# Kernel optimization log

Measured on AMD Instinct MI355X. Metric: run time of the kernel, lower is better.

Reference implementation:

```python
import jax, jax.numpy as jnp
import numpy as np

BN_EPS = 1e-5
HEADS = 8

def _bn(y, gamma, beta, mean, var):
    # eval-mode BatchNorm2d over channel axis 1; y: [B,C,H,W]
    scale = gamma / jnp.sqrt(var + BN_EPS)
    shift = beta - mean * scale
    return y * scale[None, :, None, None] + shift[None, :, None, None]

def setup_inputs() -> dict:
    key = jax.random.key(0)
    ks = jax.random.split(key, 12)
    B, C, H, W = 16, 256, 64, 64
    x = jax.random.normal(ks[0], (B, C, H, W), jnp.float32)
    qkv_w = jax.random.normal(ks[1], (3 * C, C), jnp.float32) * 0.05
    qkv_gamma = jax.random.uniform(ks[2], (3 * C,), jnp.float32, 0.5, 1.5)
    qkv_beta = jax.random.normal(ks[3], (3 * C,), jnp.float32) * 0.1
    qkv_mean = jax.random.normal(ks[4], (3 * C,), jnp.float32) * 0.1
    qkv_var = jax.random.uniform(ks[5], (3 * C,), jnp.float32, 0.5, 1.5)
    proj_w = jax.random.normal(ks[6], (C, C), jnp.float32) * 0.05
    proj_gamma = jax.random.uniform(ks[7], (C,), jnp.float32, 0.5, 1.5)
    proj_beta = jax.random.normal(ks[8], (C,), jnp.float32) * 0.1
    proj_mean = jax.random.normal(ks[9], (C,), jnp.float32) * 0.1
    proj_var = jax.random.uniform(ks[10], (C,), jnp.float32, 0.5, 1.5)
    return {"x": x, "qkv_w": qkv_w, "qkv_gamma": qkv_gamma, "qkv_beta": qkv_beta,
            "qkv_mean": qkv_mean, "qkv_var": qkv_var, "proj_w": proj_w,
            "proj_gamma": proj_gamma, "proj_beta": proj_beta,
            "proj_mean": proj_mean, "proj_var": proj_var}

def reference(x, qkv_w, qkv_gamma, qkv_beta, qkv_mean, qkv_var,
              proj_w, proj_gamma, proj_beta, proj_mean, proj_var):
    B, C, H, W = x.shape
    hd = C // HEADS  # head_dim
    # 1x1 conv (no bias) + BN
    qkv = jnp.einsum('bchw,oc->bohw', x, qkv_w)
    qkv = _bn(qkv, qkv_gamma, qkv_beta, qkv_mean, qkv_var)
    q, k, v = jnp.split(qkv, 3, axis=1)
    N = H * W
    q = q.reshape(B, HEADS, hd, N)
    k = k.reshape(B, HEADS, hd, N)
    v = v.reshape(B, HEADS, hd, N)
    q = jax.nn.softmax(q, axis=-1)   # over tokens
    k = jax.nn.softmax(k, axis=-2)   # over head_dim
    context = jnp.einsum('bhdn,bhen->bhde', k, v)   # [B,h,d,d]
    out = jnp.einsum('bhdn,bhde->bhen', q, context) # [B,h,d,N]
    out = out.reshape(B, C, H, W)
    out = jnp.einsum('bchw,oc->bohw', out, proj_w)
    out = _bn(out, proj_gamma, proj_beta, proj_mean, proj_var)
    return out
```

## Files before the change

kernel.cpp:

```cpp
#include <hip/hip_runtime.h>

typedef unsigned short ushort_t;
typedef unsigned int u32;
typedef short short8 __attribute__((ext_vector_type(8)));
typedef short short4_t __attribute__((ext_vector_type(4)));
typedef float f32x4 __attribute__((ext_vector_type(4)));
typedef float f32x16 __attribute__((ext_vector_type(16)));

#define NTOK 4096
#define NCOLS 65536
#define CIN 256

__device__ __forceinline__ float b2f(ushort_t u) {
    union { unsigned int i; float f; } v; v.i = ((unsigned int)u) << 16; return v.f;
}
__device__ __forceinline__ ushort_t f2b(float f) {
    union { float f; unsigned int i; } v; v.f = f;
    unsigned int r = v.i + 0x7FFFu + ((v.i >> 16) & 1u);
    return (ushort_t)(r >> 16);
}

__device__ __forceinline__ void gl_lds16(const ushort_t* g, ushort_t* l) {
    __builtin_amdgcn_global_load_lds(
        (const __attribute__((address_space(1))) u32*)(const void*)g,
        (__attribute__((address_space(3))) u32*)(void*)l,
        16, 0, 0);
}

__global__ __launch_bounds__(256) void cvt_w(const float* __restrict__ wq,
                                             const float* __restrict__ wp,
                                             ushort_t* __restrict__ wqb,
                                             ushort_t* __restrict__ wpb,
                                             float* __restrict__ scz) {
    int i = blockIdx.x * 256 + threadIdx.x;
    if (i < 768 * 256) wqb[i] = f2b(wq[i]);
    else               wpb[i - 768 * 256] = f2b(wp[i - 768 * 256]);
    if (i < 131072) scz[i] = 0.f;
}

__global__ __launch_bounds__(256) void transpose_x(const float* __restrict__ x,
                                                   ushort_t* __restrict__ xt) {
    __shared__ ushort_t lds[64 * 264];
    int tid = threadIdx.x;
    int g0 = blockIdx.x * 64;
    int b = g0 >> 12, n0 = g0 & 4095;
    const float* src = x + (size_t)b * (CIN * NTOK);
    int tn = tid & 63, cg = tid >> 6;
    for (int c4 = 0; c4 < 64; c4++) {
        int c = c4 * 4 + cg;
        lds[tn * 264 + c] = f2b(src[(size_t)c * NTOK + n0 + tn]);
    }
    __syncthreads();
    int tok = tid >> 2, c8 = (tid & 3) * 8;
    ushort_t* dst = xt + (size_t)(g0 + tok) * CIN + c8;
#pragma unroll
    for (int j = 0; j < 8; j++)
        *(short8*)(dst + j * 32) = *(const short8*)&lds[tok * 264 + c8 + j * 32];
}

__global__ __launch_bounds__(256) void gemm128(const ushort_t* __restrict__ W,
                                               const ushort_t* __restrict__ Xc,
                                               const float* __restrict__ gamma,
                                               const float* __restrict__ beta,
                                               const float* __restrict__ mean,
                                               const float* __restrict__ var,
                                               ushort_t* __restrict__ out_b,
                                               float* __restrict__ out_f, int mode) {
    __shared__ __align__(16) ushort_t lA[128 * 32];
    __shared__ __align__(16) ushort_t lB[128 * 32];
    int tid = threadIdx.x;
    int wave = tid >> 6, lane = tid & 63;
    int l15 = lane & 15, q = lane >> 4;
    int mh = wave >> 1, nh = wave & 1;
    int m0 = blockIdx.y * 128, colb = blockIdx.x * 128;

    f32x4 acc[4][4];
#pragma unroll
    for (int i = 0; i < 4; i++)
#pragma unroll
        for (int j = 0; j < 4; j++)
#pragma unroll
            for (int r = 0; r < 4; r++) acc[i][j][r] = 0.f;

    const ushort_t* gA0 = W  + (size_t)(m0 +      (tid >> 2)) * CIN + (tid & 3) * 8;
    const ushort_t* gA1 = W  + (size_t)(m0 + 64 + (tid >> 2)) * CIN + (tid & 3) * 8;
    const ushort_t* gB0 = Xc + (size_t)(colb +      (tid >> 2)) * CIN + (tid & 3) * 8;
    const ushort_t* gB1 = Xc + (size_t)(colb + 64 + (tid >> 2)) * CIN + (tid & 3) * 8;
    ushort_t* la0 = &lA[tid * 8];
    ushort_t* la1 = &lA[2048 + tid * 8];
    ushort_t* lb0 = &lB[tid * 8];
    ushort_t* lb1 = &lB[2048 + tid * 8];

    for (int k0 = 0; k0 < CIN; k0 += 32) {
        gl_lds16(gA0 + k0, la0);
        gl_lds16(gA1 + k0, la1);
        gl_lds16(gB0 + k0, lb0);
        gl_lds16(gB1 + k0, lb1);
        __syncthreads();
        short8 af[4], bf[4];
#pragma unroll
        for (int i = 0; i < 4; i++) {
            af[i] = *(const short8*)&lA[(mh * 64 + i * 16 + l15) * 32 + q * 8];
            bf[i] = *(const short8*)&lB[(nh * 64 + i * 16 + l15) * 32 + q * 8];
        }
#pragma unroll
        for (int mi = 0; mi < 4; mi++)
#pragma unroll
            for (int ni = 0; ni < 4; ni++)
                acc[mi][ni] = __builtin_amdgcn_mfma_f32_16x16x32_bf16(af[mi], bf[ni],
                                                                      acc[mi][ni], 0, 0, 0);
        __syncthreads();
    }

    int col_l = colb + nh * 64 + l15;
#pragma unroll
    for (int mi = 0; mi < 4; mi++) {
#pragma unroll
        for (int r = 0; r < 4; r++) {
            int m = m0 + mh * 64 + mi * 16 + q * 4 + r;
            float sc = gamma[m] * rsqrtf(var[m] + 1e-5f);
            float sh = beta[m] - mean[m] * sc;
#pragma unroll
            for (int ni = 0; ni < 4; ni++) {
                float val = acc[mi][ni][r] * sc + sh;
                int col = col_l + ni * 16;
                if (mode == 0) {
                    out_b[(size_t)m * NCOLS + col] = f2b(val);
                } else {
                    int bb = col >> 12, n = col & 4095;
                    out_f[(size_t)bb * (CIN * NTOK) + (size_t)m * NTOK + n] = val;
                }
            }
        }
    }
}

__global__ __launch_bounds__(256) void qsum_ker(const ushort_t* __restrict__ qkv,
                                                float* __restrict__ qsums) {
    int tid = threadIdx.x, wave = tid >> 6, lane = tid & 63;
    int rid = blockIdx.x * 4 + wave;
    int c = rid >> 4, b = rid & 15;
    const ushort_t* row = qkv + (size_t)c * NCOLS + b * NTOK;
    float s = 0.f;
#pragma unroll
    for (int j = 0; j < 8; j++) {
        short8 pk = *(const short8*)(row + j * 512 + lane * 8);
#pragma unroll
        for (int i = 0; i < 8; i++) s += __expf(b2f((ushort_t)pk[i]));
    }
    for (int off = 1; off < 64; off <<= 1) s += __shfl_xor(s, off);
    if (lane == 0) qsums[c * 16 + b] = s;
}

__global__ __launch_bounds__(256) void ctx_ker(const ushort_t* __restrict__ qkv,
                                               float* __restrict__ ctxbuf) {
    int sl = blockIdx.x, bh = blockIdx.y;
    int b = bh >> 3, h = bh & 7;
    int tid = threadIdx.x, wave = tid >> 6, lane = tid & 63;
    int l31 = lane & 31, l5 = lane >> 5;
    int col0 = b * NTOK + sl * 512 + wave * 128;
    const ushort_t* krow = qkv + (size_t)(256 + h * 32 + l31) * NCOLS + col0 + l5 * 8;
    const ushort_t* vrow = qkv + (size_t)(512 + h * 32 + l31) * NCOLS + col0 + l5 * 8;
    f32x16 acc;
#pragma unroll
    for (int i = 0; i < 16; i++) acc[i] = 0.f;
#pragma unroll
    for (int st = 0; st < 8; st++) {
        short8 kf = *(const short8*)(krow + st * 16);
        short8 vf = *(const short8*)(vrow + st * 16);
        short8 af;
#pragma unroll
        for (int j = 0; j < 8; j++) {
            float e = __expf(b2f((ushort_t)kf[j]));
            float t = e;
            t += __shfl_xor(t, 1);
            t += __shfl_xor(t, 2);
            t += __shfl_xor(t, 4);
            t += __shfl_xor(t, 8);
            t += __shfl_xor(t, 16);
            af[j] = (short)f2b(__fdividef(e, t));
        }
        acc = __builtin_amdgcn_mfma_f32_32x32x16_bf16(af, vf, acc, 0, 0, 0);
    }
    __shared__ float red[4][1024];
#pragma unroll
    for (int r = 0; r < 16; r++) {
        int d = (r & 3) + 8 * (r >> 2) + 4 * l5;
        red[wave][d * 32 + l31] = acc[r];
    }
    __syncthreads();
    int i0 = tid * 4;
#pragma unroll
    for (int i = 0; i < 4; i++) {
        int idx = i0 + i;
        float v = red[0][idx] + red[1][idx] + red[2][idx] + red[3][idx];
        atomicAdd(ctxbuf + (size_t)bh * 1024 + idx, v);
    }
}

__global__ __launch_bounds__(256) void out_ker(const ushort_t* __restrict__ qkv,
                                               const float* __restrict__ ctxbuf,
                                               const float* __restrict__ qsums,
                                               ushort_t* __restrict__ attT) {
    int sl = blockIdx.x, bh = blockIdx.y;
    int b = bh >> 3, h = bh & 7;
    int tid = threadIdx.x, wave = tid >> 6, lane = tid & 63;
    int l31 = lane & 31, l5 = lane >> 5;
    __shared__ __align__(16) ushort_t ctxT[32 * 40];
    __shared__ __align__(16) ushort_t qT[256 * 40];
    __shared__ __align__(16) ushort_t obuf[4][32 * 40];

#pragma unroll
    for (int i = 0; i < 4; i++) {
        int idx = tid * 4 + i;
        int d = idx >> 5, e = idx & 31;
        ctxT[e * 40 + d] = f2b(ctxbuf[(size_t)bh * 1024 + idx]);
    }
    __syncthreads();
    short8 a0 = *(const short8*)(ctxT + l31 * 40 + l5 * 8);
    short8 a1 = *(const short8*)(ctxT + l31 * 40 + 16 + l5 * 8);

    const ushort_t* qbase = qkv + (size_t)(h * 32) * NCOLS;
    int segbase = b * NTOK + sl * 512;
    int d = tid & 31, t8 = (tid >> 5) * 8;
    float sq = 1.f / qsums[(h * 32 + d) * 16 + b];

    for (int nc = 0; nc < 2; nc++) {
        int gcol0 = segbase + nc * 256;
#pragma unroll
        for (int jj = 0; jj < 4; jj++) {
            int tok8 = jj * 64 + t8;
            short8 pk = *(const short8*)(qbase + (size_t)d * NCOLS + gcol0 + tok8);
#pragma unroll
            for (int j = 0; j < 8; j++)
                qT[(tok8 + j) * 40 + d] = f2b(__expf(b2f((ushort_t)pk[j])) * sq);
        }
        __syncthreads();
#pragma unroll
        for (int ti = 0; ti < 2; ti++) {
            int tok0 = (wave + ti * 4) * 32;
            f32x16 acc;
#pragma unroll
            for (int i = 0; i < 16; i++) acc[i] = 0.f;
            short8 b0 = *(const short8*)(qT + (size_t)(tok0 + l31) * 40 + l5 * 8);
            short8 b1 = *(const short8*)(qT + (size_t)(tok0 + l31) * 40 + 16 + l5 * 8);
            acc = __builtin_amdgcn_mfma_f32_32x32x16_bf16(a0, b0, acc, 0, 0, 0);
            acc = __builtin_amdgcn_mfma_f32_32x32x16_bf16(a1, b1, acc, 0, 0, 0);
#pragma unroll
            for (int r = 0; r < 16; r++) {
                int e = (r & 3) + 8 * (r >> 2) + 4 * l5;
                obuf[wave][l31 * 40 + e] = f2b(acc[r]);
            }
            __syncthreads();
            {
                int tok = lane >> 1, half = lane & 1;
                const ushort_t* srcp = &obuf[wave][tok * 40 + half * 16];
                short8 r0 = *(const short8*)srcp;
                short8 r1 = *(const short8*)(srcp + 8);
                size_t g = (size_t)(gcol0 + tok0 + tok) * 256 + h * 32 + half * 16;
                *(short8*)(attT + g) = r0;
                *(short8*)(attT + g + 8) = r1;
            }
            __syncthreads();
        }
        __syncthreads();
    }
}

extern "C" void kernel_launch(void* const* d_in, const int* in_sizes, int n_in,
                              void* d_out, int out_size, void* d_ws, size_t ws_size,
                              hipStream_t stream) {
    const float* x          = (const float*)d_in[0];
    const float* qkv_w      = (const float*)d_in[1];
    const float* qkv_gamma  = (const float*)d_in[2];
    const float* qkv_beta   = (const float*)d_in[3];
    const float* qkv_mean   = (const float*)d_in[4];
    const float* qkv_var    = (const float*)d_in[5];
    const float* proj_w     = (const float*)d_in[6];
    const float* proj_gamma = (const float*)d_in[7];
    const float* proj_beta  = (const float*)d_in[8];
    const float* proj_mean  = (const float*)d_in[9];
    const float* proj_var   = (const float*)d_in[10];

    ushort_t* wqb = (ushort_t*)d_ws;
    ushort_t* wpb = wqb + 768 * 256;
    ushort_t* xt  = wpb + 256 * 256;
    ushort_t* qkv = xt + (size_t)NCOLS * CIN;
    float* out    = (float*)d_out;
    float* ctxbuf = (float*)d_out;
    float* qsums  = ctxbuf + 131072;

    cvt_w<<<1024, 256, 0, stream>>>(qkv_w, proj_w, wqb, wpb, ctxbuf);
    transpose_x<<<1024, 256, 0, stream>>>(x, xt);
    gemm128<<<dim3(512, 6), 256, 0, stream>>>(wqb, xt, qkv_gamma, qkv_beta,
                                              qkv_mean, qkv_var, qkv, nullptr, 0);
    qsum_ker<<<1024, 256, 0, stream>>>(qkv, qsums);
    ctx_ker<<<dim3(8, 128), 256, 0, stream>>>(qkv, ctxbuf);
    out_ker<<<dim3(8, 128), 256, 0, stream>>>(qkv, ctxbuf, qsums, xt);
    gemm128<<<dim3(512, 2), 256, 0, stream>>>(wpb, xt, proj_gamma, proj_beta,
                                              proj_mean, proj_var, nullptr, out, 1);
}
```

Before: 298.5 us.

## Keep weight tiles in registers and stage full-K activation tiles in LDS

The 1x1-conv GEMM kernel changes from a 128x128 tile that streams both operands through LDS in 32-wide K steps, with two barriers per step. It now uses 512-thread blocks covering 256 output channels. Each wave holds its whole 64xK weight slice in registers, and the block loads a full 128-token by 256-K activation tile into LDS in one shot, covering two column tiles per block. This removes the per-K-step barriers and the repeated weight reloads, at the cost of heavy register use (128 VGPRs for weight fragments plus accumulators), 64 KB of LDS per block, and no overlap between loads and MFMA work.

```diff
diff --git a/kernel.cpp b/kernel.cpp
--- a/kernel.cpp
+++ b/kernel.cpp
@@ -3,7 +3,6 @@
 typedef unsigned short ushort_t;
 typedef unsigned int u32;
 typedef short short8 __attribute__((ext_vector_type(8)));
-typedef short short4_t __attribute__((ext_vector_type(4)));
 typedef float f32x4 __attribute__((ext_vector_type(4)));
 typedef float f32x16 __attribute__((ext_vector_type(16)));
 
@@ -58,77 +57,83 @@
         *(short8*)(dst + j * 32) = *(const short8*)&lds[tok * 264 + c8 + j * 32];
 }
 
-__global__ __launch_bounds__(256) void gemm128(const ushort_t* __restrict__ W,
-                                               const ushort_t* __restrict__ Xc,
-                                               const float* __restrict__ gamma,
-                                               const float* __restrict__ beta,
-                                               const float* __restrict__ mean,
-                                               const float* __restrict__ var,
-                                               ushort_t* __restrict__ out_b,
-                                               float* __restrict__ out_f, int mode) {
-    __shared__ __align__(16) ushort_t lA[128 * 32];
-    __shared__ __align__(16) ushort_t lB[128 * 32];
+__global__ __launch_bounds__(512, 2) void gemmW(const ushort_t* __restrict__ W,
+                                                const ushort_t* __restrict__ Xc,
+                                                const float* __restrict__ gamma,
+                                                const float* __restrict__ beta,
+                                                const float* __restrict__ mean,
+                                                const float* __restrict__ var,
+                                                ushort_t* __restrict__ out_b,
+                                                float* __restrict__ out_f, int mode) {
+    __shared__ __align__(16) ushort_t lB[32768];
     int tid = threadIdx.x;
     int wave = tid >> 6, lane = tid & 63;
     int l15 = lane & 15, q = lane >> 4;
-    int mh = wave >> 1, nh = wave & 1;
-    int m0 = blockIdx.y * 128, colb = blockIdx.x * 128;
-
-    f32x4 acc[4][4];
-#pragma unroll
-    for (int i = 0; i < 4; i++)
-#pragma unroll
-        for (int j = 0; j < 4; j++)
-#pragma unroll
-            for (int r = 0; r < 4; r++) acc[i][j][r] = 0.f;
-
-    const ushort_t* gA0 = W  + (size_t)(m0 +      (tid >> 2)) * CIN + (tid & 3) * 8;
-    const ushort_t* gA1 = W  + (size_t)(m0 + 64 + (tid >> 2)) * CIN + (tid & 3) * 8;
-    const ushort_t* gB0 = Xc + (size_t)(colb +      (tid >> 2)) * CIN + (tid & 3) * 8;
-    const ushort_t* gB1 = Xc + (size_t)(colb + 64 + (tid >> 2)) * CIN + (tid & 3) * 8;
-    ushort_t* la0 = &lA[tid * 8];
-    ushort_t* la1 = &lA[2048 + tid * 8];
-    ushort_t* lb0 = &lB[tid * 8];
-    ushort_t* lb1 = &lB[2048 + tid * 8];
-
-    for (int k0 = 0; k0 < CIN; k0 += 32) {
-        gl_lds16(gA0 + k0, la0);
-        gl_lds16(gA1 + k0, la1);
-        gl_lds16(gB0 + k0, lb0);
-        gl_lds16(gB1 + k0, lb1);
-        __syncthreads();
-        short8 af[4], bf[4];
+    int mq = wave >> 1, nq = wave & 1;
+    int m0 = blockIdx.y * 256;
+    int mrow = m0 + mq * 64;
+
+    short8 afr[8][4];
+#pragma unroll
+    for (int ks = 0; ks < 8; ks++)
+#pragma unroll
+        for (int i = 0; i < 4; i++)
+            afr[ks][i] = *(const short8*)(W + (size_t)(mrow + i * 16 + l15) * CIN
+                                            + ks * 32 + q * 8);
+
+    const ushort_t* gB = Xc + (size_t)(blockIdx.x * 256 + (tid >> 2)) * CIN
+                            + (tid & 3) * 8;
+
+    for (int ct = 0; ct < 2; ct++) {
+        if (ct) __builtin_amdgcn_s_barrier();
+        const ushort_t* gBt = gB + ct * 128 * CIN;
+#pragma unroll
+        for (int ks = 0; ks < 8; ks++)
+            gl_lds16(gBt + ks * 32, &lB[ks * 4096 + tid * 8]);
+        asm volatile("s_waitcnt vmcnt(0)" ::: "memory");
+        __builtin_amdgcn_s_barrier();
+
+        f32x4 acc[4][4];
+#pragma unroll
+        for (int i = 0; i < 4; i++)
+#pragma unroll
+            for (int j = 0; j < 4; j++)
+#pragma unroll
+                for (int r = 0; r < 4; r++) acc[i][j][r] = 0.f;
+
+#pragma unroll
+        for (int ks = 0; ks < 8; ks++) {
+            short8 bf[4];
+#pragma unroll
+            for (int nj = 0; nj < 4; nj++)
+                bf[nj] = *(const short8*)&lB[ks * 4096
+                                             + (nq * 64 + nj * 16 + l15) * 32 + q * 8];
+#pragma unroll
+            for (int i = 0; i < 4; i++)
+#pragma unroll
+                for (int nj = 0; nj < 4; nj++)
+                    acc[i][nj] = __builtin_amdgcn_mfma_f32_16x16x32_bf16(
+                        afr[ks][i], bf[nj], acc[i][nj], 0, 0, 0);
+        }
+
+        int colb = blockIdx.x * 256 + ct * 128;
 #pragma unroll
         for (int i = 0; i < 4; i++) {
-            af[i] = *(const short8*)&lA[(mh * 64 + i * 16 + l15) * 32 + q * 8];
-            bf[i] = *(const short8*)&lB[(nh * 64 + i * 16 + l15) * 32 + q * 8];
-        }
-#pragma unroll
-        for (int mi = 0; mi < 4; mi++)
-#pragma unroll
-            for (int ni = 0; ni < 4; ni++)
-                acc[mi][ni] = __builtin_amdgcn_mfma_f32_16x16x32_bf16(af[mi], bf[ni],
-                                                                      acc[mi][ni], 0, 0, 0);
-        __syncthreads();
-    }
-
-    int col_l = colb + nh * 64 + l15;
-#pragma unroll
-    for (int mi = 0; mi < 4; mi++) {
-#pragma unroll
-        for (int r = 0; r < 4; r++) {
-            int m = m0 + mh * 64 + mi * 16 + q * 4 + r;
-            float sc = gamma[m] * rsqrtf(var[m] + 1e-5f);
-            float sh = beta[m] - mean[m] * sc;
-#pragma unroll
-            for (int ni = 0; ni < 4; ni++) {
-                float val = acc[mi][ni][r] * sc + sh;
-                int col = col_l + ni * 16;
-                if (mode == 0) {
-                    out_b[(size_t)m * NCOLS + col] = f2b(val);
-                } else {
-                    int bb = col >> 12, n = col & 4095;
-                    out_f[(size_t)bb * (CIN * NTOK) + (size_t)m * NTOK + n] = val;
+#pragma unroll
+            for (int r = 0; r < 4; r++) {
+                int m = mrow + i * 16 + q * 4 + r;
+                float sc = gamma[m] * rsqrtf(var[m] + 1e-5f);
+                float sh = beta[m] - mean[m] * sc;
+#pragma unroll
+                for (int nj = 0; nj < 4; nj++) {
+                    float val = acc[i][nj][r] * sc + sh;
+                    int col = colb + nq * 64 + nj * 16 + l15;
+                    if (mode == 0) {
+                        out_b[(size_t)m * NCOLS + col] = f2b(val);
+                    } else {
+                        int bb = col >> 12, n = col & 4095;
+                        out_f[(size_t)bb * (CIN * NTOK) + (size_t)m * NTOK + n] = val;
+                    }
                 }
             }
         }
@@ -292,11 +297,11 @@
 
     cvt_w<<<1024, 256, 0, stream>>>(qkv_w, proj_w, wqb, wpb, ctxbuf);
     transpose_x<<<1024, 256, 0, stream>>>(x, xt);
-    gemm128<<<dim3(512, 6), 256, 0, stream>>>(wqb, xt, qkv_gamma, qkv_beta,
-                                              qkv_mean, qkv_var, qkv, nullptr, 0);
+    gemmW<<<dim3(256, 3), 512, 0, stream>>>(wqb, xt, qkv_gamma, qkv_beta,
+                                            qkv_mean, qkv_var, qkv, nullptr, 0);
     qsum_ker<<<1024, 256, 0, stream>>>(qkv, qsums);
     ctx_ker<<<dim3(8, 128), 256, 0, stream>>>(qkv, ctxbuf);
     out_ker<<<dim3(8, 128), 256, 0, stream>>>(qkv, ctxbuf, qsums, xt);
-    gemm128<<<dim3(512, 2), 256, 0, stream>>>(wpb, xt, proj_gamma, proj_beta,
-                                              proj_mean, proj_var, nullptr, out, 1);
-}
+    gemmW<<<dim3(256, 1), 512, 0, stream>>>(wpb, xt, proj_gamma, proj_beta,
+                                            proj_mean, proj_var, nullptr, out, 1);
+}
```

After: 384.6 us. 28.8% more time.

## Fuse weight conversion into transpose and q-softmax sums into QKV GEMM epilogue

Applied to the files above, without the earlier changes.

Merges the weight-conversion kernel into the x-transpose kernel and removes the separate qsum pass. The QKV GEMM epilogue now accumulates exp of the bf16 q values, reduces across 16 lanes, and atomically adds per-row, per-batch partial sums into qsums. The zeroing range is extended so qsums is cleared by the prep kernel. This saves two launches and a full re-read of the q rows, at the cost of atomics and extra exp work inside the GEMM epilogue.

```diff
diff --git a/kernel.cpp b/kernel.cpp
--- a/kernel.cpp
+++ b/kernel.cpp
@@ -3,7 +3,6 @@
 typedef unsigned short ushort_t;
 typedef unsigned int u32;
 typedef short short8 __attribute__((ext_vector_type(8)));
-typedef short short4_t __attribute__((ext_vector_type(4)));
 typedef float f32x4 __attribute__((ext_vector_type(4)));
 typedef float f32x16 __attribute__((ext_vector_type(16)));
 
@@ -27,21 +26,21 @@
         16, 0, 0);
 }
 
-__global__ __launch_bounds__(256) void cvt_w(const float* __restrict__ wq,
-                                             const float* __restrict__ wp,
-                                             ushort_t* __restrict__ wqb,
-                                             ushort_t* __restrict__ wpb,
-                                             float* __restrict__ scz) {
-    int i = blockIdx.x * 256 + threadIdx.x;
+__global__ __launch_bounds__(256) void prep_x(const float* __restrict__ x,
+                                              ushort_t* __restrict__ xt,
+                                              const float* __restrict__ wq,
+                                              const float* __restrict__ wp,
+                                              ushort_t* __restrict__ wqb,
+                                              ushort_t* __restrict__ wpb,
+                                              float* __restrict__ scz) {
+    __shared__ ushort_t lds[64 * 264];
+    int tid = threadIdx.x;
+
+    int i = blockIdx.x * 256 + tid;
     if (i < 768 * 256) wqb[i] = f2b(wq[i]);
     else               wpb[i - 768 * 256] = f2b(wp[i - 768 * 256]);
-    if (i < 131072) scz[i] = 0.f;
-}
-
-__global__ __launch_bounds__(256) void transpose_x(const float* __restrict__ x,
-                                                   ushort_t* __restrict__ xt) {
-    __shared__ ushort_t lds[64 * 264];
-    int tid = threadIdx.x;
+    if (i < 135168) scz[i] = 0.f;
+
     int g0 = blockIdx.x * 64;
     int b = g0 >> 12, n0 = g0 & 4095;
     const float* src = x + (size_t)b * (CIN * NTOK);
@@ -65,7 +64,8 @@
                                                const float* __restrict__ mean,
                                                const float* __restrict__ var,
                                                ushort_t* __restrict__ out_b,
-                                               float* __restrict__ out_f, int mode) {
+                                               float* __restrict__ out_f,
+                                               float* __restrict__ qsums, int mode) {
     __shared__ __align__(16) ushort_t lA[128 * 32];
     __shared__ __align__(16) ushort_t lB[128 * 32];
     int tid = threadIdx.x;
@@ -113,6 +113,7 @@
     }
 
     int col_l = colb + nh * 64 + l15;
+    int bq = colb >> 12;
 #pragma unroll
     for (int mi = 0; mi < 4; mi++) {
 #pragma unroll
@@ -120,36 +121,29 @@
             int m = m0 + mh * 64 + mi * 16 + q * 4 + r;
             float sc = gamma[m] * rsqrtf(var[m] + 1e-5f);
             float sh = beta[m] - mean[m] * sc;
+            float qs = 0.f;
 #pragma unroll
             for (int ni = 0; ni < 4; ni++) {
                 float val = acc[mi][ni][r] * sc + sh;
                 int col = col_l + ni * 16;
                 if (mode == 0) {
-                    out_b[(size_t)m * NCOLS + col] = f2b(val);
+                    ushort_t bv = f2b(val);
+                    out_b[(size_t)m * NCOLS + col] = bv;
+                    if (m < 256) qs += __expf(b2f(bv));
                 } else {
                     int bb = col >> 12, n = col & 4095;
                     out_f[(size_t)bb * (CIN * NTOK) + (size_t)m * NTOK + n] = val;
                 }
             }
-        }
-    }
-}
-
-__global__ __launch_bounds__(256) void qsum_ker(const ushort_t* __restrict__ qkv,
-                                                float* __restrict__ qsums) {
-    int tid = threadIdx.x, wave = tid >> 6, lane = tid & 63;
-    int rid = blockIdx.x * 4 + wave;
-    int c = rid >> 4, b = rid & 15;
-    const ushort_t* row = qkv + (size_t)c * NCOLS + b * NTOK;
-    float s = 0.f;
-#pragma unroll
-    for (int j = 0; j < 8; j++) {
-        short8 pk = *(const short8*)(row + j * 512 + lane * 8);
-#pragma unroll
-        for (int i = 0; i < 8; i++) s += __expf(b2f((ushort_t)pk[i]));
-    }
-    for (int off = 1; off < 64; off <<= 1) s += __shfl_xor(s, off);
-    if (lane == 0) qsums[c * 16 + b] = s;
+            if (mode == 0 && m < 256) {
+                qs += __shfl_xor(qs, 1);
+                qs += __shfl_xor(qs, 2);
+                qs += __shfl_xor(qs, 4);
+                qs += __shfl_xor(qs, 8);
+                if (l15 == 0) atomicAdd(&qsums[m * 16 + bq], qs);
+            }
+        }
+    }
 }
 
 __global__ __launch_bounds__(256) void ctx_ker(const ushort_t* __restrict__ qkv,
@@ -290,13 +284,13 @@
     float* ctxbuf = (float*)d_out;
     float* qsums  = ctxbuf + 131072;
 
-    cvt_w<<<1024, 256, 0, stream>>>(qkv_w, proj_w, wqb, wpb, ctxbuf);
-    transpose_x<<<1024, 256, 0, stream>>>(x, xt);
+    prep_x<<<1024, 256, 0, stream>>>(x, xt, qkv_w, proj_w, wqb, wpb, ctxbuf);
     gemm128<<<dim3(512, 6), 256, 0, stream>>>(wqb, xt, qkv_gamma, qkv_beta,
-                                              qkv_mean, qkv_var, qkv, nullptr, 0);
-    qsum_ker<<<1024, 256, 0, stream>>>(qkv, qsums);
+                                              qkv_mean, qkv_var, qkv, nullptr,
+                                              qsums, 0);
     ctx_ker<<<dim3(8, 128), 256, 0, stream>>>(qkv, ctxbuf);
     out_ker<<<dim3(8, 128), 256, 0, stream>>>(qkv, ctxbuf, qsums, xt);
     gemm128<<<dim3(512, 2), 256, 0, stream>>>(wpb, xt, proj_gamma, proj_beta,
-                                              proj_mean, proj_var, nullptr, out, 1);
-}
+                                              proj_mean, proj_var, nullptr, out,
+                                              nullptr, 1);
+}
```

New measurement: 356.1 us. 19.3% more time.

## Precompute k-softmax reciprocals, replace context atomics with partial buffers, fuse prep kernels

Applied to the files above, without the earlier changes.

The weight conversion and x transpose kernels are merged into one prep kernel. The per-token k softmax denominators now come from extra blocks added to the q-sum kernel, which store reciprocals so ctx_ker no longer needs five shuffles and a divide per element. ctx_ker writes per-slice partial contexts instead of using atomicAdd, and out_ker sums the 8 partials, which also removes the zeroing pass. The cost is an extra pass that reads K and an extra 2 MB reciprocal buffer, plus larger scratch use in the output buffer.

```diff
diff --git a/kernel.cpp b/kernel.cpp
--- a/kernel.cpp
+++ b/kernel.cpp
@@ -3,7 +3,6 @@
 typedef unsigned short ushort_t;
 typedef unsigned int u32;
 typedef short short8 __attribute__((ext_vector_type(8)));
-typedef short short4_t __attribute__((ext_vector_type(4)));
 typedef float f32x4 __attribute__((ext_vector_type(4)));
 typedef float f32x16 __attribute__((ext_vector_type(16)));
 
@@ -27,21 +26,19 @@
         16, 0, 0);
 }
 
-__global__ __launch_bounds__(256) void cvt_w(const float* __restrict__ wq,
-                                             const float* __restrict__ wp,
-                                             ushort_t* __restrict__ wqb,
-                                             ushort_t* __restrict__ wpb,
-                                             float* __restrict__ scz) {
-    int i = blockIdx.x * 256 + threadIdx.x;
+__global__ __launch_bounds__(256) void prep_x(const float* __restrict__ x,
+                                              ushort_t* __restrict__ xt,
+                                              const float* __restrict__ wq,
+                                              const float* __restrict__ wp,
+                                              ushort_t* __restrict__ wqb,
+                                              ushort_t* __restrict__ wpb) {
+    __shared__ ushort_t lds[64 * 264];
+    int tid = threadIdx.x;
+
+    int i = blockIdx.x * 256 + tid;
     if (i < 768 * 256) wqb[i] = f2b(wq[i]);
     else               wpb[i - 768 * 256] = f2b(wp[i - 768 * 256]);
-    if (i < 131072) scz[i] = 0.f;
-}
-
-__global__ __launch_bounds__(256) void transpose_x(const float* __restrict__ x,
-                                                   ushort_t* __restrict__ xt) {
-    __shared__ ushort_t lds[64 * 264];
-    int tid = threadIdx.x;
+
     int g0 = blockIdx.x * 64;
     int b = g0 >> 12, n0 = g0 & 4095;
     const float* src = x + (size_t)b * (CIN * NTOK);
@@ -135,25 +132,50 @@
     }
 }
 
-__global__ __launch_bounds__(256) void qsum_ker(const ushort_t* __restrict__ qkv,
-                                                float* __restrict__ qsums) {
-    int tid = threadIdx.x, wave = tid >> 6, lane = tid & 63;
-    int rid = blockIdx.x * 4 + wave;
-    int c = rid >> 4, b = rid & 15;
-    const ushort_t* row = qkv + (size_t)c * NCOLS + b * NTOK;
-    float s = 0.f;
-#pragma unroll
-    for (int j = 0; j < 8; j++) {
-        short8 pk = *(const short8*)(row + j * 512 + lane * 8);
-#pragma unroll
-        for (int i = 0; i < 8; i++) s += __expf(b2f((ushort_t)pk[i]));
-    }
-    for (int off = 1; off < 64; off <<= 1) s += __shfl_xor(s, off);
-    if (lane == 0) qsums[c * 16 + b] = s;
+__global__ __launch_bounds__(256) void sum_ker(const ushort_t* __restrict__ qkv,
+                                               float* __restrict__ qsums,
+                                               float* __restrict__ rsums) {
+    int tid = threadIdx.x;
+    if (blockIdx.x < 1024) {
+        int wave = tid >> 6, lane = tid & 63;
+        int rid = blockIdx.x * 4 + wave;
+        int c = rid >> 4, b = rid & 15;
+        const ushort_t* row = qkv + (size_t)c * NCOLS + b * NTOK;
+        float s = 0.f;
+#pragma unroll
+        for (int j = 0; j < 8; j++) {
+            short8 pk = *(const short8*)(row + j * 512 + lane * 8);
+#pragma unroll
+            for (int i = 0; i < 8; i++) s += __expf(b2f((ushort_t)pk[i]));
+        }
+        for (int off = 1; off < 64; off <<= 1) s += __shfl_xor(s, off);
+        if (lane == 0) qsums[c * 16 + b] = s;
+    } else {
+        int kb = blockIdx.x - 1024;
+        int bh = kb >> 1, half = kb & 1;
+        int b = bh >> 3, h = bh & 7;
+        const ushort_t* base = qkv + (size_t)(256 + h * 32) * NCOLS
+                                   + b * NTOK + half * 2048 + tid * 8;
+        float s[8];
+#pragma unroll
+        for (int j = 0; j < 8; j++) s[j] = 0.f;
+        for (int ch = 0; ch < 32; ch++) {
+            short8 kk = *(const short8*)(base + (size_t)ch * NCOLS);
+#pragma unroll
+            for (int j = 0; j < 8; j++) s[j] += __expf(b2f((ushort_t)kk[j]));
+        }
+        float* rp = rsums + (size_t)bh * NTOK + half * 2048 + tid * 8;
+        f32x4 r0, r1;
+#pragma unroll
+        for (int j = 0; j < 4; j++) { r0[j] = 1.f / s[j]; r1[j] = 1.f / s[j + 4]; }
+        *(f32x4*)rp = r0;
+        *(f32x4*)(rp + 4) = r1;
+    }
 }
 
 __global__ __launch_bounds__(256) void ctx_ker(const ushort_t* __restrict__ qkv,
-                                               float* __restrict__ ctxbuf) {
+                                               const float* __restrict__ rsums,
+                                               float* __restrict__ ctxpart) {
     int sl = blockIdx.x, bh = blockIdx.y;
     int b = bh >> 3, h = bh & 7;
     int tid = threadIdx.x, wave = tid >> 6, lane = tid & 63;
@@ -161,6 +183,7 @@
     int col0 = b * NTOK + sl * 512 + wave * 128;
     const ushort_t* krow = qkv + (size_t)(256 + h * 32 + l31) * NCOLS + col0 + l5 * 8;
     const ushort_t* vrow = qkv + (size_t)(512 + h * 32 + l31) * NCOLS + col0 + l5 * 8;
+    const float* rsp = rsums + (size_t)bh * NTOK + sl * 512 + wave * 128 + l5 * 8;
     f32x16 acc;
 #pragma unroll
     for (int i = 0; i < 16; i++) acc[i] = 0.f;
@@ -168,18 +191,15 @@
     for (int st = 0; st < 8; st++) {
         short8 kf = *(const short8*)(krow + st * 16);
         short8 vf = *(const short8*)(vrow + st * 16);
+        f32x4 ra = *(const f32x4*)(rsp + st * 16);
+        f32x4 rb = *(const f32x4*)(rsp + st * 16 + 4);
         short8 af;
 #pragma unroll
-        for (int j = 0; j < 8; j++) {
-            float e = __expf(b2f((ushort_t)kf[j]));
-            float t = e;
-            t += __shfl_xor(t, 1);
-            t += __shfl_xor(t, 2);
-            t += __shfl_xor(t, 4);
-            t += __shfl_xor(t, 8);
-            t += __shfl_xor(t, 16);
-            af[j] = (short)f2b(__fdividef(e, t));
-        }
+        for (int j = 0; j < 4; j++)
+            af[j] = (short)f2b(__expf(b2f((ushort_t)kf[j])) * ra[j]);
+#pragma unroll
+        for (int j = 0; j < 4; j++)
+            af[j + 4] = (short)f2b(__expf(b2f((ushort_t)kf[j + 4])) * rb[j]);
         acc = __builtin_amdgcn_mfma_f32_32x32x16_bf16(af, vf, acc, 0, 0, 0);
     }
     __shared__ float red[4][1024];
@@ -190,16 +210,15 @@
     }
     __syncthreads();
     int i0 = tid * 4;
-#pragma unroll
-    for (int i = 0; i < 4; i++) {
-        int idx = i0 + i;
-        float v = red[0][idx] + red[1][idx] + red[2][idx] + red[3][idx];
-        atomicAdd(ctxbuf + (size_t)bh * 1024 + idx, v);
-    }
+    f32x4 vv;
+#pragma unroll
+    for (int i = 0; i < 4; i++)
+        vv[i] = red[0][i0 + i] + red[1][i0 + i] + red[2][i0 + i] + red[3][i0 + i];
+    *(f32x4*)(ctxpart + ((size_t)sl * 128 + bh) * 1024 + i0) = vv;
 }
 
 __global__ __launch_bounds__(256) void out_ker(const ushort_t* __restrict__ qkv,
-                                               const float* __restrict__ ctxbuf,
+                                               const float* __restrict__ ctxpart,
                                                const float* __restrict__ qsums,
                                                ushort_t* __restrict__ attT) {
     int sl = blockIdx.x, bh = blockIdx.y;
@@ -210,11 +229,20 @@
     __shared__ __align__(16) ushort_t qT[256 * 40];
     __shared__ __align__(16) ushort_t obuf[4][32 * 40];
 
-#pragma unroll
-    for (int i = 0; i < 4; i++) {
-        int idx = tid * 4 + i;
-        int d = idx >> 5, e = idx & 31;
-        ctxT[e * 40 + d] = f2b(ctxbuf[(size_t)bh * 1024 + idx]);
+    {
+        int i0 = tid * 4;
+        f32x4 v;
+#pragma unroll
+        for (int i = 0; i < 4; i++) v[i] = 0.f;
+#pragma unroll
+        for (int s = 0; s < 8; s++)
+            v += *(const f32x4*)(ctxpart + ((size_t)s * 128 + bh) * 1024 + i0);
+#pragma unroll
+        for (int i = 0; i < 4; i++) {
+            int idx = i0 + i;
+            int d = idx >> 5, e = idx & 31;
+            ctxT[e * 40 + d] = f2b(v[i]);
+        }
     }
     __syncthreads();
     short8 a0 = *(const short8*)(ctxT + l31 * 40 + l5 * 8);
@@ -286,17 +314,17 @@
     ushort_t* wpb = wqb + 768 * 256;
     ushort_t* xt  = wpb + 256 * 256;
     ushort_t* qkv = xt + (size_t)NCOLS * CIN;
-    float* out    = (float*)d_out;
-    float* ctxbuf = (float*)d_out;
-    float* qsums  = ctxbuf + 131072;
-
-    cvt_w<<<1024, 256, 0, stream>>>(qkv_w, proj_w, wqb, wpb, ctxbuf);
-    transpose_x<<<1024, 256, 0, stream>>>(x, xt);
+    float* out     = (float*)d_out;
+    float* ctxpart = (float*)d_out;
+    float* rsums   = ctxpart + 8 * 128 * 1024;
+    float* qsums   = rsums + 128 * NTOK;
+
+    prep_x<<<1024, 256, 0, stream>>>(x, xt, qkv_w, proj_w, wqb, wpb);
     gemm128<<<dim3(512, 6), 256, 0, stream>>>(wqb, xt, qkv_gamma, qkv_beta,
                                               qkv_mean, qkv_var, qkv, nullptr, 0);
-    qsum_ker<<<1024, 256, 0, stream>>>(qkv, qsums);
-    ctx_ker<<<dim3(8, 128), 256, 0, stream>>>(qkv, ctxbuf);
-    out_ker<<<dim3(8, 128), 256, 0, stream>>>(qkv, ctxbuf, qsums, xt);
+    sum_ker<<<1280, 256, 0, stream>>>(qkv, qsums, rsums);
+    ctx_ker<<<dim3(8, 128), 256, 0, stream>>>(qkv, rsums, ctxpart);
+    out_ker<<<dim3(8, 128), 256, 0, stream>>>(qkv, ctxpart, qsums, xt);
     gemm128<<<dim3(512, 2), 256, 0, stream>>>(wpb, xt, proj_gamma, proj_beta,
                                               proj_mean, proj_var, nullptr, out, 1);
 }
```

Measured after the change: 292.2 us. -2.1%, faster.
